# Performance work log

Measured on AMD Instinct MI355X. Metric: run time of the kernel, lower is better.

The kernel has to match this reference:

```python
import jax, jax.numpy as jnp
import numpy as np

N_USERS = 200_000
N_ITEMS = 100_000
EMB = 64
N_EDGES = 5_000_000
N_LAYERS = 3


def setup_inputs() -> dict:
    key = jax.random.key(0)
    k1, k2, k3, k4, k5 = jax.random.split(key, 5)
    emb_user = jax.random.normal(k1, (N_USERS, EMB), dtype=jnp.float32) * 0.1
    emb_item = jax.random.normal(k2, (N_ITEMS, EMB), dtype=jnp.float32) * 0.1
    n_nodes = N_USERS + N_ITEMS
    edge_row = jax.random.randint(k3, (N_EDGES,), 0, n_nodes, dtype=jnp.int32)
    edge_col = jax.random.randint(k4, (N_EDGES,), 0, n_nodes, dtype=jnp.int32)
    # normalized adjacency values (positive, < 1), stand-in for D^-1/2 A D^-1/2
    edge_val = jax.random.uniform(k5, (N_EDGES,), dtype=jnp.float32)
    return {"emb_user": emb_user, "emb_item": emb_item,
            "edge_val": edge_val, "edge_row": edge_row, "edge_col": edge_col}


def reference(emb_user, emb_item, edge_val, edge_row, edge_col):
    n_users = emb_user.shape[0]
    n_nodes = n_users + emb_item.shape[0]
    # 0th-layer embedding matrix: cat(user, item)  [N, D]
    x = jnp.concatenate([emb_user, emb_item], axis=0)
    layers = [x]
    for _ in range(N_LAYERS):
        # SpMM: out[r] += val * x[c] for each edge (r, c)
        x = jax.ops.segment_sum(edge_val[:, None] * x[edge_col], edge_row,
                                num_segments=n_nodes)
        layers.append(x)
    # layer combination: mean over all layers
    agg = jnp.mean(jnp.stack(layers, axis=0), axis=0)
    return agg[:n_users], agg[n_users:]
```

## Files before the change

kernel.cpp:

```cpp
#include <hip/hip_runtime.h>

#define N_USERS 200000
#define N_ITEMS 100000
#define N_NODES 300000
#define EMB     64
#define N_EDGES 5000000

typedef float f32x4 __attribute__((ext_vector_type(4)));
typedef _Float16 f16;
typedef f16 f16x4 __attribute__((ext_vector_type(4)));

struct alignas(8) Edge { int col; float val; };
struct alignas(8) SRec { unsigned int rc; float val; };

#define BSHIFT 11
#define BROWS  (1 << BSHIFT)
#define NBUCK  ((N_NODES + BROWS - 1) >> BSHIFT)
#define CAP    40960
#define BIN_CHUNK 16384
#define COLMASK 0x7FFFFu

__global__ __launch_bounds__(256) void fused_init_bin_kernel(
    const float* __restrict__ user, const float* __restrict__ item,
    f16* __restrict__ x, float* __restrict__ out,
    const int4* __restrict__ row4, const int4* __restrict__ col4,
    const float4* __restrict__ val4,
    int* __restrict__ bcursor, SRec* __restrict__ stage, int bin_blocks)
{
    int t = threadIdx.x;
    if ((int)blockIdx.x < bin_blocks) {
        __shared__ int hist[NBUCK];
        __shared__ int base_[NBUCK];
        const int Q = N_EDGES / 4;
        long q0 = (long)blockIdx.x * (BIN_CHUNK / 4);

        for (int k = t; k < NBUCK; k += 256) hist[k] = 0;
        __syncthreads();

        #pragma unroll
        for (int k = 0; k < 16; ++k) {
            long q = q0 + k * 256 + t;
            if (q < Q) {
                int4 r = row4[q];
                atomicAdd(&hist[r.x >> BSHIFT], 1);
                atomicAdd(&hist[r.y >> BSHIFT], 1);
                atomicAdd(&hist[r.z >> BSHIFT], 1);
                atomicAdd(&hist[r.w >> BSHIFT], 1);
            }
        }
        __syncthreads();
        for (int k = t; k < NBUCK; k += 256) {
            int h = hist[k];
            base_[k] = h ? atomicAdd(&bcursor[k], h) : 0;
            hist[k] = 0;
        }
        __syncthreads();
        #pragma unroll
        for (int k = 0; k < 16; ++k) {
            long q = q0 + k * 256 + t;
            if (q < Q) {
                int4 r = row4[q]; int4 c = col4[q]; float4 v = val4[q];
                int   rr[4] = {r.x, r.y, r.z, r.w};
                int   cc[4] = {c.x, c.y, c.z, c.w};
                float vv[4] = {v.x, v.y, v.z, v.w};
                #pragma unroll
                for (int j = 0; j < 4; ++j) {
                    int b   = rr[j] >> BSHIFT;
                    int pos = base_[b] + atomicAdd(&hist[b], 1);
                    SRec s;
                    s.rc  = ((unsigned)(rr[j] & (BROWS - 1)) << 19) | (unsigned)cc[j];
                    s.val = vv[j];
                    stage[(size_t)b * CAP + pos] = s;
                }
            }
        }
    } else {
        const int nu4 = N_USERS * EMB / 4;
        const int nt4 = N_NODES * EMB / 4;
        int i = ((int)blockIdx.x - bin_blocks) * 256 + t;
        if (i >= nt4) return;
        float4 vv = (i < nu4) ? reinterpret_cast<const float4*>(user)[i]
                              : reinterpret_cast<const float4*>(item)[i - nu4];
        f16x4 hx = {(f16)vv.x, (f16)vv.y, (f16)vv.z, (f16)vv.w};
        reinterpret_cast<f16x4*>(x)[i] = hx;
        f32x4 ov = {vv.x, vv.y, vv.z, vv.w};
        __builtin_nontemporal_store(ov, reinterpret_cast<f32x4*>(out) + i);
    }
}

__global__ __launch_bounds__(1024) void bucket_scan_scatter_kernel(
    const SRec* __restrict__ stage, const int* __restrict__ bsize,
    int* __restrict__ start, Edge* __restrict__ packed)
{
    __shared__ int sizes[NBUCK];
    __shared__ int cnt[BROWS];
    __shared__ int cur[BROWS];
    __shared__ int sc[1024];
    __shared__ int sbase;

    int b    = blockIdx.x;
    int t    = threadIdx.x;
    int row0 = b << BSHIFT;
    int rows = N_NODES - row0; if (rows > BROWS) rows = BROWS;

    if (t < NBUCK) sizes[t] = bsize[t];
    for (int i = t; i < BROWS; i += 1024) cnt[i] = 0;
    __syncthreads();
    if (t == 0) {
        int s = 0;
        for (int k = 0; k < b; ++k) s += sizes[k];
        sbase = s;
    }
    __syncthreads();
    const int  base = sbase;
    const int  size = sizes[b];
    const SRec* seg = stage + (size_t)b * CAP;

    for (int e = t; e < size; e += 1024)
        atomicAdd(&cnt[seg[e].rc >> 19], 1);
    __syncthreads();

    int a0 = cnt[2 * t], a1 = cnt[2 * t + 1];
    int s01 = a0 + a1;
    sc[t] = s01;
    __syncthreads();
    for (int ofs = 1; ofs < 1024; ofs <<= 1) {
        int v = (t >= ofs) ? sc[t - ofs] : 0;
        __syncthreads();
        sc[t] += v;
        __syncthreads();
    }
    int ex = sc[t] - s01;
    cur[2 * t]     = base + ex;
    cur[2 * t + 1] = base + ex + a0;
    __syncthreads();

    for (int i = t; i < rows; i += 1024) start[row0 + i] = cur[i];
    if (b == NBUCK - 1 && t == 0) start[N_NODES] = N_EDGES;
    __syncthreads();

    for (int e = t; e < size; e += 1024) {
        SRec srec = seg[e];
        int pos = atomicAdd(&cur[srec.rc >> 19], 1);
        Edge p; p.col = (int)(srec.rc & COLMASK); p.val = srec.val;
        packed[pos] = p;
    }
}

__global__ __launch_bounds__(256, 4) void spmm_csr_kernel(
    const f16* __restrict__ x, const Edge* __restrict__ packed,
    const int* __restrict__ start,
    f16* __restrict__ y, float* __restrict__ out, float scale, int write_y)
{
    int g = blockIdx.x * (256 / 16) + (threadIdx.x >> 4);
    if (g >= N_NODES) return;
    const int lane16 = threadIdx.x & 15;
    const int d      = lane16 * 4;
    const int gbase  = threadIdx.x & 48;

    int beg = start[g];
    int end = start[g + 1];
    float4 acc = {0.f, 0.f, 0.f, 0.f};

    for (int jb = beg; jb < end; jb += 16) {
        Edge ed; ed.col = 0; ed.val = 0.f;
        if (jb + lane16 < end) ed = packed[jb + lane16];

        int   cols[16];
        float vals[16];
        #pragma unroll
        for (int k = 0; k < 16; ++k) {
            cols[k] = __shfl(ed.col, gbase + k, 64);
            vals[k] = __shfl(ed.val, gbase + k, 64);
        }

        f16x4 xv[16];
        #pragma unroll
        for (int k = 0; k < 16; ++k) {
            xv[k] = *reinterpret_cast<const f16x4*>(
                x + (size_t)cols[k] * EMB + d);
        }

        #pragma unroll
        for (int k = 0; k < 16; ++k) {
            acc.x += vals[k] * (float)xv[k].x;
            acc.y += vals[k] * (float)xv[k].y;
            acc.z += vals[k] * (float)xv[k].z;
            acc.w += vals[k] * (float)xv[k].w;
        }
    }

    if (write_y) {
        f16x4 hy = {(f16)acc.x, (f16)acc.y, (f16)acc.z, (f16)acc.w};
        *reinterpret_cast<f16x4*>(y + (size_t)g * EMB + d) = hy;
    }

    f32x4* op = reinterpret_cast<f32x4*>(out + (size_t)g * EMB + d);
    f32x4 o = __builtin_nontemporal_load(op);
    o.x = (o.x + acc.x) * scale;
    o.y = (o.y + acc.y) * scale;
    o.z = (o.z + acc.z) * scale;
    o.w = (o.w + acc.w) * scale;
    __builtin_nontemporal_store(o, op);
}

__global__ __launch_bounds__(256) void init_kernel(
    const float* __restrict__ user, const float* __restrict__ item,
    float* __restrict__ x, float* __restrict__ out)
{
    const int nu4 = N_USERS * EMB / 4;
    const int nt4 = N_NODES * EMB / 4;
    int i = blockIdx.x * blockDim.x + threadIdx.x;
    if (i >= nt4) return;
    float4 v = (i < nu4) ? reinterpret_cast<const float4*>(user)[i]
                         : reinterpret_cast<const float4*>(item)[i - nu4];
    reinterpret_cast<float4*>(x)[i]   = v;
    reinterpret_cast<float4*>(out)[i] = v;
}

__global__ __launch_bounds__(256) void spmm_atomic_kernel(
    const float* __restrict__ x, const float* __restrict__ val,
    const int* __restrict__ row, const int* __restrict__ col,
    float* __restrict__ y)
{
    int t = blockIdx.x * blockDim.x + threadIdx.x;
    int e = t >> 4;
    if (e >= N_EDGES) return;
    int d = (t & 15) * 4;
    int   r = row[e];
    int   c = col[e];
    float v = val[e];
    float4 xv = *reinterpret_cast<const float4*>(x + c * EMB + d);
    float* yp = y + r * EMB + d;
    unsafeAtomicAdd(yp + 0, v * xv.x);
    unsafeAtomicAdd(yp + 1, v * xv.y);
    unsafeAtomicAdd(yp + 2, v * xv.z);
    unsafeAtomicAdd(yp + 3, v * xv.w);
}

__global__ __launch_bounds__(256) void addscale_kernel(
    const float* __restrict__ xl, float* __restrict__ out, float scale)
{
    const int nt4 = N_NODES * EMB / 4;
    int i = blockIdx.x * blockDim.x + threadIdx.x;
    if (i >= nt4) return;
    float4 a = reinterpret_cast<float4*>(out)[i];
    float4 b = reinterpret_cast<const float4*>(xl)[i];
    a.x = (a.x + b.x) * scale;
    a.y = (a.y + b.y) * scale;
    a.z = (a.z + b.z) * scale;
    a.w = (a.w + b.w) * scale;
    reinterpret_cast<float4*>(out)[i] = a;
}

extern "C" void kernel_launch(void* const* d_in, const int* in_sizes, int n_in,
                              void* d_out, int out_size, void* d_ws, size_t ws_size,
                              hipStream_t stream) {
    const float* emb_user = (const float*)d_in[0];
    const float* emb_item = (const float*)d_in[1];
    const float* edge_val = (const float*)d_in[2];
    const int*   edge_row = (const int*)d_in[3];
    const int*   edge_col = (const int*)d_in[4];
    float* out = (float*)d_out;

    const size_t node_elems = (size_t)N_NODES * EMB;
    char* ws = (char*)d_ws;

    const size_t off_bufA    = 0;
    const size_t off_bufB    = off_bufA + node_elems * sizeof(float);
    const size_t off_packed  = off_bufB + node_elems * sizeof(float);
    const size_t off_start   = off_packed + (size_t)N_EDGES * sizeof(Edge);
    const size_t off_bcursor = off_start + (N_NODES + 4) * sizeof(int);
    const size_t needed      = off_bcursor + (NBUCK + 4) * sizeof(int);

    const int nt4       = N_NODES * EMB / 4;
    const int el_blocks = (nt4 + 255) / 256;
    const int e_blocks  = (N_EDGES + 255) / 256;

    static_assert((size_t)NBUCK * CAP * sizeof(SRec) <= (size_t)N_NODES * EMB * sizeof(float),
                  "stage must fit in bufB");

    if (ws_size >= needed) {
        f16*  bufA    = (f16*) (ws + off_bufA);
        f16*  bufB    = (f16*) (ws + off_bufB);
        Edge* packed  = (Edge*)(ws + off_packed);
        int*  start   = (int*) (ws + off_start);
        int*  bcursor = (int*) (ws + off_bcursor);
        SRec* stage   = (SRec*)(ws + off_bufB);

        hipMemsetAsync(bcursor, 0, (NBUCK + 4) * sizeof(int), stream);

        const int bin_blocks = (N_EDGES + BIN_CHUNK - 1) / BIN_CHUNK;
        fused_init_bin_kernel<<<bin_blocks + el_blocks, 256, 0, stream>>>(
            emb_user, emb_item, bufA, out,
            (const int4*)edge_row, (const int4*)edge_col, (const float4*)edge_val,
            bcursor, stage, bin_blocks);

        bucket_scan_scatter_kernel<<<NBUCK, 1024, 0, stream>>>(
            stage, bcursor, start, packed);

        const int row_blocks = (N_NODES + 15) / 16;
        f16* cur = bufA;
        f16* nxt = bufB;
        for (int layer = 0; layer < 3; ++layer) {
            spmm_csr_kernel<<<row_blocks, 256, 0, stream>>>(
                cur, packed, start, nxt, out,
                (layer == 2) ? 0.25f : 1.0f,
                (layer == 2) ? 0 : 1);
            f16* tmp = cur; cur = nxt; nxt = tmp;
        }
    } else {
        float* fbufA = (float*)(ws + off_bufA);
        float* fbufB = (float*)(ws + off_bufB);
        init_kernel<<<el_blocks, 256, 0, stream>>>(emb_user, emb_item, fbufA, out);
        const int ew_blocks = (N_EDGES * 16 + 255) / 256;
        float* cur = fbufA;
        float* nxt = fbufB;
        for (int layer = 0; layer < 3; ++layer) {
            hipMemsetAsync(nxt, 0, node_elems * sizeof(float), stream);
            spmm_atomic_kernel<<<ew_blocks, 256, 0, stream>>>(
                cur, edge_val, edge_row, edge_col, nxt);
            addscale_kernel<<<el_blocks, 256, 0, stream>>>(
                nxt, out, (layer == 2) ? 0.25f : 1.0f);
            float* tmp = cur; cur = nxt; nxt = tmp;
        }
    }
}
```

Before: 655.9 us.

## Split edge arrays, store fp16 edge weights, defer layer mean to final SpMM

Replaces the packed (col,val) edge struct with separate int column and fp16 value arrays, which shrinks the per-edge bytes read on each of the three SpMM passes. It also keeps every layer's fp16 embedding in its own buffer and computes the layer mean once in the last SpMM pass, so the fp32 output no longer gets a read-modify-write per layer or an initial write. Bucket size is halved so each scatter thread handles one row counter, which simplifies the scan. The cost is fp16 rounding of the edge weights and of layer 0 in the final mean, with some accuracy risk.

Result: no change. 651.6 us (-0.7%).

```diff
diff --git a/kernel.cpp b/kernel.cpp
--- a/kernel.cpp
+++ b/kernel.cpp
@@ -10,19 +10,18 @@
 typedef _Float16 f16;
 typedef f16 f16x4 __attribute__((ext_vector_type(4)));
 
-struct alignas(8) Edge { int col; float val; };
 struct alignas(8) SRec { unsigned int rc; float val; };
 
-#define BSHIFT 11
+#define BSHIFT 10
 #define BROWS  (1 << BSHIFT)
 #define NBUCK  ((N_NODES + BROWS - 1) >> BSHIFT)
-#define CAP    40960
+#define CAP    20480
 #define BIN_CHUNK 16384
 #define COLMASK 0x7FFFFu
 
 __global__ __launch_bounds__(256) void fused_init_bin_kernel(
     const float* __restrict__ user, const float* __restrict__ item,
-    f16* __restrict__ x, float* __restrict__ out,
+    f16* __restrict__ x0,
     const int4* __restrict__ row4, const int4* __restrict__ col4,
     const float4* __restrict__ val4,
     int* __restrict__ bcursor, SRec* __restrict__ stage, int bin_blocks)
@@ -82,18 +81,15 @@
         float4 vv = (i < nu4) ? reinterpret_cast<const float4*>(user)[i]
                               : reinterpret_cast<const float4*>(item)[i - nu4];
         f16x4 hx = {(f16)vv.x, (f16)vv.y, (f16)vv.z, (f16)vv.w};
-        reinterpret_cast<f16x4*>(x)[i] = hx;
-        f32x4 ov = {vv.x, vv.y, vv.z, vv.w};
-        __builtin_nontemporal_store(ov, reinterpret_cast<f32x4*>(out) + i);
+        reinterpret_cast<f16x4*>(x0)[i] = hx;
     }
 }
 
 __global__ __launch_bounds__(1024) void bucket_scan_scatter_kernel(
     const SRec* __restrict__ stage, const int* __restrict__ bsize,
-    int* __restrict__ start, Edge* __restrict__ packed)
+    int* __restrict__ start, int* __restrict__ pcol, f16* __restrict__ pval)
 {
     __shared__ int sizes[NBUCK];
-    __shared__ int cnt[BROWS];
     __shared__ int cur[BROWS];
     __shared__ int sc[1024];
     __shared__ int sbase;
@@ -104,7 +100,7 @@
     int rows = N_NODES - row0; if (rows > BROWS) rows = BROWS;
 
     if (t < NBUCK) sizes[t] = bsize[t];
-    for (int i = t; i < BROWS; i += 1024) cnt[i] = 0;
+    cur[t] = 0;
     __syncthreads();
     if (t == 0) {
         int s = 0;
@@ -117,12 +113,11 @@
     const SRec* seg = stage + (size_t)b * CAP;
 
     for (int e = t; e < size; e += 1024)
-        atomicAdd(&cnt[seg[e].rc >> 19], 1);
-    __syncthreads();
-
-    int a0 = cnt[2 * t], a1 = cnt[2 * t + 1];
-    int s01 = a0 + a1;
-    sc[t] = s01;
+        atomicAdd(&cur[seg[e].rc >> 19], 1);
+    __syncthreads();
+
+    int a = cur[t];
+    sc[t] = a;
     __syncthreads();
     for (int ofs = 1; ofs < 1024; ofs <<= 1) {
         int v = (t >= ofs) ? sc[t - ofs] : 0;
@@ -130,27 +125,27 @@
         sc[t] += v;
         __syncthreads();
     }
-    int ex = sc[t] - s01;
-    cur[2 * t]     = base + ex;
-    cur[2 * t + 1] = base + ex + a0;
-    __syncthreads();
-
-    for (int i = t; i < rows; i += 1024) start[row0 + i] = cur[i];
+    cur[t] = base + sc[t] - a;
+    __syncthreads();
+
+    if (t < rows) start[row0 + t] = cur[t];
     if (b == NBUCK - 1 && t == 0) start[N_NODES] = N_EDGES;
     __syncthreads();
 
     for (int e = t; e < size; e += 1024) {
         SRec srec = seg[e];
         int pos = atomicAdd(&cur[srec.rc >> 19], 1);
-        Edge p; p.col = (int)(srec.rc & COLMASK); p.val = srec.val;
-        packed[pos] = p;
+        pcol[pos] = (int)(srec.rc & COLMASK);
+        pval[pos] = (f16)srec.val;
     }
 }
 
 __global__ __launch_bounds__(256, 4) void spmm_csr_kernel(
-    const f16* __restrict__ x, const Edge* __restrict__ packed,
-    const int* __restrict__ start,
-    f16* __restrict__ y, float* __restrict__ out, float scale, int write_y)
+    const f16* __restrict__ x, const int* __restrict__ pcol,
+    const f16* __restrict__ pval, const int* __restrict__ start,
+    f16* __restrict__ y,
+    const f16* __restrict__ xa, const f16* __restrict__ xb,
+    float* __restrict__ out, int mode)
 {
     int g = blockIdx.x * (256 / 16) + (threadIdx.x >> 4);
     if (g >= N_NODES) return;
@@ -163,15 +158,18 @@
     float4 acc = {0.f, 0.f, 0.f, 0.f};
 
     for (int jb = beg; jb < end; jb += 16) {
-        Edge ed; ed.col = 0; ed.val = 0.f;
-        if (jb + lane16 < end) ed = packed[jb + lane16];
+        int   mycol = 0; float myval = 0.f;
+        if (jb + lane16 < end) {
+            mycol = pcol[jb + lane16];
+            myval = (float)pval[jb + lane16];
+        }
 
         int   cols[16];
         float vals[16];
         #pragma unroll
         for (int k = 0; k < 16; ++k) {
-            cols[k] = __shfl(ed.col, gbase + k, 64);
-            vals[k] = __shfl(ed.val, gbase + k, 64);
+            cols[k] = __shfl(mycol, gbase + k, 64);
+            vals[k] = __shfl(myval, gbase + k, 64);
         }
 
         f16x4 xv[16];
@@ -190,18 +188,21 @@
         }
     }
 
-    if (write_y) {
+    const size_t rofs = (size_t)g * EMB + d;
+    if (mode == 0) {
         f16x4 hy = {(f16)acc.x, (f16)acc.y, (f16)acc.z, (f16)acc.w};
-        *reinterpret_cast<f16x4*>(y + (size_t)g * EMB + d) = hy;
-    }
-
-    f32x4* op = reinterpret_cast<f32x4*>(out + (size_t)g * EMB + d);
-    f32x4 o = __builtin_nontemporal_load(op);
-    o.x = (o.x + acc.x) * scale;
-    o.y = (o.y + acc.y) * scale;
-    o.z = (o.z + acc.z) * scale;
-    o.w = (o.w + acc.w) * scale;
-    __builtin_nontemporal_store(o, op);
+        *reinterpret_cast<f16x4*>(y + rofs) = hy;
+    } else {
+        f16x4 v0 = *reinterpret_cast<const f16x4*>(xa + rofs);
+        f16x4 v1 = *reinterpret_cast<const f16x4*>(xb + rofs);
+        f16x4 v2 = *reinterpret_cast<const f16x4*>(x  + rofs);
+        f32x4 o;
+        o.x = 0.25f * ((float)v0.x + (float)v1.x + (float)v2.x + acc.x);
+        o.y = 0.25f * ((float)v0.y + (float)v1.y + (float)v2.y + acc.y);
+        o.z = 0.25f * ((float)v0.z + (float)v1.z + (float)v2.z + acc.z);
+        o.w = 0.25f * ((float)v0.w + (float)v1.w + (float)v2.w + acc.w);
+        __builtin_nontemporal_store(o, reinterpret_cast<f32x4*>(out + rofs));
+    }
 }
 
 __global__ __launch_bounds__(256) void init_kernel(
@@ -268,8 +269,9 @@
 
     const size_t off_bufA    = 0;
     const size_t off_bufB    = off_bufA + node_elems * sizeof(float);
-    const size_t off_packed  = off_bufB + node_elems * sizeof(float);
-    const size_t off_start   = off_packed + (size_t)N_EDGES * sizeof(Edge);
+    const size_t off_pcol    = off_bufB + node_elems * sizeof(float);
+    const size_t off_pval    = off_pcol + (size_t)N_EDGES * sizeof(int);
+    const size_t off_start   = off_pval + (size_t)N_EDGES * sizeof(f16);
     const size_t off_bcursor = off_start + (N_NODES + 4) * sizeof(int);
     const size_t needed      = off_bcursor + (NBUCK + 4) * sizeof(int);
 
@@ -278,12 +280,14 @@
     const int e_blocks  = (N_EDGES + 255) / 256;
 
     static_assert((size_t)NBUCK * CAP * sizeof(SRec) <= (size_t)N_NODES * EMB * sizeof(float),
-                  "stage must fit in bufB");
+                  "stage must fit in bufB region");
 
     if (ws_size >= needed) {
-        f16*  bufA    = (f16*) (ws + off_bufA);
-        f16*  bufB    = (f16*) (ws + off_bufB);
-        Edge* packed  = (Edge*)(ws + off_packed);
+        f16*  x0buf   = (f16*) (ws + off_bufA);
+        f16*  x2buf   = (f16*) (ws + off_bufA) + node_elems;
+        f16*  x1buf   = (f16*) (ws + off_bufB);
+        int*  pcol    = (int*) (ws + off_pcol);
+        f16*  pval    = (f16*) (ws + off_pval);
         int*  start   = (int*) (ws + off_start);
         int*  bcursor = (int*) (ws + off_bcursor);
         SRec* stage   = (SRec*)(ws + off_bufB);
@@ -292,23 +296,20 @@
 
         const int bin_blocks = (N_EDGES + BIN_CHUNK - 1) / BIN_CHUNK;
         fused_init_bin_kernel<<<bin_blocks + el_blocks, 256, 0, stream>>>(
-            emb_user, emb_item, bufA, out,
+            emb_user, emb_item, x0buf,
             (const int4*)edge_row, (const int4*)edge_col, (const float4*)edge_val,
             bcursor, stage, bin_blocks);
 
         bucket_scan_scatter_kernel<<<NBUCK, 1024, 0, stream>>>(
-            stage, bcursor, start, packed);
+            stage, bcursor, start, pcol, pval);
 
         const int row_blocks = (N_NODES + 15) / 16;
-        f16* cur = bufA;
-        f16* nxt = bufB;
-        for (int layer = 0; layer < 3; ++layer) {
-            spmm_csr_kernel<<<row_blocks, 256, 0, stream>>>(
-                cur, packed, start, nxt, out,
-                (layer == 2) ? 0.25f : 1.0f,
-                (layer == 2) ? 0 : 1);
-            f16* tmp = cur; cur = nxt; nxt = tmp;
-        }
+        spmm_csr_kernel<<<row_blocks, 256, 0, stream>>>(
+            x0buf, pcol, pval, start, x1buf, nullptr, nullptr, nullptr, 0);
+        spmm_csr_kernel<<<row_blocks, 256, 0, stream>>>(
+            x1buf, pcol, pval, start, x2buf, nullptr, nullptr, nullptr, 0);
+        spmm_csr_kernel<<<row_blocks, 256, 0, stream>>>(
+            x2buf, pcol, pval, start, nullptr, x0buf, x1buf, out, 1);
     } else {
         float* fbufA = (float*)(ws + off_bufA);
         float* fbufB = (float*)(ws + off_bufB);
```
